# Kernel tuning notes

Hardware: AMD Instinct MI355X
Metric: run time of the kernel (lower is better)

Reference implementation:

```python
import jax, jax.numpy as jnp
import numpy as np

B = 1024      # batch of videos
T = 32768     # max snippets per video


def setup_inputs() -> dict:
    key = jax.random.key(0)
    k1, k2, k3 = jax.random.split(key, 3)
    # sigmoid-like scores in (0,1) as BCELoss expects probabilities
    scores = jax.random.uniform(k1, (B, T), dtype=jnp.float32, minval=1e-4, maxval=1.0 - 1e-4)
    label = jax.random.uniform(k2, (B,), dtype=jnp.float32)
    seqlen = jax.random.randint(k3, (B,), 1, T + 1, dtype=jnp.int32)
    return {"scores": scores, "label": label, "seqlen": seqlen}


def reference(scores, label, seqlen):
    # fwd_topk with cfg.k == -1: per-sample k_i = seqlen_i // 16 + 1,
    # mean of the top-k_i scores within the valid prefix scores[i, :seqlen_i],
    # followed by BCELoss against label.
    _, t = scores.shape
    pos = jnp.arange(t)[None, :]                      # [1, T]
    valid = pos < seqlen[:, None]                     # [B, T] ragged-length mask
    # push invalid tail to -inf so descending sort puts valid values first
    masked = jnp.where(valid, scores, -jnp.inf)
    srt = -jnp.sort(-masked, axis=1)                  # descending sort, valid prefix first
    # zero out the (-inf) tail; exactly seqlen_i leading entries are valid
    srt = jnp.where(valid, srt, 0.0)
    csum = jnp.cumsum(srt, axis=1)                    # prefix sums of sorted scores
    k = seqlen // 16 + 1                              # per-sample k, always <= seqlen
    topk_sum = jnp.take_along_axis(csum, (k - 1)[:, None], axis=1)[:, 0]
    vl_scores = topk_sum / k.astype(scores.dtype)     # mean of top-k per sample, [B]
    # BCELoss (mean reduction)
    loss = -jnp.mean(label * jnp.log(vl_scores) + (1.0 - label) * jnp.log1p(-vl_scores))
    return loss
```

## Files before the change

### kernel.cpp

```cpp
#include <hip/hip_runtime.h>
#include <math.h>

#define NB    2048
#define BLK   1024
#define NCH   256
#define CHW   (NB / NCH)
#define FIXS  1048576.0f
#define SUMMASK ((1ULL << 44) - 1)


__global__ void zero_out_kernel(float* __restrict__ out) { out[0] = 0.0f; }

__global__ __launch_bounds__(BLK) void topk_bce_kernel(
    const float* __restrict__ scores,
    const float* __restrict__ label,
    const int*   __restrict__ seqlen,
    float*       __restrict__ out,
    int T, int B)
{
    __shared__ unsigned long long hist[NB];
    __shared__ int                sc_cnt[NCH];
    __shared__ unsigned long long sc_sum[NCH];
    __shared__ int s_t, s_acc;
    __shared__ unsigned long long s_vs;

    const int row = blockIdx.x;
    const int tid = threadIdx.x;
    const int n   = seqlen[row];
    const int k   = (n >> 4) + 1;
    const float* rp   = scores + (size_t)row * (size_t)T;
    const float4* rp4 = (const float4*)rp;
    const int n4 = n >> 2;

    float lo  = 0.875f;
    float mul = 16384.0f;

    for (;;) {
        for (int i = tid; i < NB; i += BLK) hist[i] = 0ULL;
        __syncthreads();

#define PUT(x) do { \
            const float _x = (x); \
            if (_x >= lo) { \
                int _b = (int)((_x - lo) * mul); \
                if (_b > NB - 1) _b = NB - 1; \
                const unsigned int _q = (unsigned int)(_x * FIXS + 0.5f); \
                atomicAdd(&hist[_b], (1ULL << 44) | (unsigned long long)_q); \
            } \
        } while (0)

        for (int j = tid; j < n4; j += BLK) {
            float4 v = rp4[j];
            PUT(v.x); PUT(v.y); PUT(v.z); PUT(v.w);
        }
        for (int j = (n4 << 2) + tid; j < n; j += BLK) PUT(rp[j]);
#undef PUT
        __syncthreads();

        if (tid < NCH) {
            int cc = 0; unsigned long long ss = 0ULL;
            const int base = tid * CHW;
            #pragma unroll
            for (int j = 0; j < CHW; ++j) {
                const unsigned long long h = hist[base + j];
                cc += (int)(h >> 44);
                ss += (h & SUMMASK);
            }
            sc_cnt[tid] = cc; sc_sum[tid] = ss;
        }
        __syncthreads();

        for (int off = 1; off < NCH; off <<= 1) {
            int vc = 0; unsigned long long vs = 0ULL;
            if (tid < NCH) {
                vc = sc_cnt[tid]; vs = sc_sum[tid];
                if (tid + off < NCH) { vc += sc_cnt[tid + off]; vs += sc_sum[tid + off]; }
            }
            __syncthreads();
            if (tid < NCH) { sc_cnt[tid] = vc; sc_sum[tid] = vs; }
            __syncthreads();
        }

        const int total = sc_cnt[0];
        if (total >= k) break;
        lo = 0.0f; mul = (float)NB;
    }

    if (tid < NCH) {
        const int SA  = sc_cnt[tid];
        const int SAn = (tid + 1 < NCH) ? sc_cnt[tid + 1] : 0;
        if (SA >= k && SAn < k) {
            s_t   = tid;
            s_acc = SAn;
            s_vs  = (tid + 1 < NCH) ? sc_sum[tid + 1] : 0ULL;
        }
    }
    __syncthreads();

    if (tid == 0) {
        const int t = s_t;
        int acc = s_acc;
        unsigned long long vs = s_vs;
        for (int j = CHW - 1; j >= 0; --j) {
            const int bin = t * CHW + j;
            const unsigned long long h = hist[bin];
            const int c = (int)(h >> 44);
            if (acc + c >= k) {
                const int r = k - acc;
                const int m = c;
                const float sum_b  = (float)(h & SUMMASK) * (1.0f / FIXS);
                const float above  = (float)vs * (1.0f / FIXS);
                const float binw   = 1.0f / mul;
                const float bin_lo = lo + (float)bin * binw;
                float topr;
                if (r >= m) {
                    topr = sum_b;
                } else if (2 * r <= m) {
                    topr = (float)r * (bin_lo + binw)
                         - binw * (float)r * (float)(r + 1) / (2.0f * (float)(m + 1));
                } else {
                    const int q2 = m - r;
                    topr = sum_b - ((float)q2 * bin_lo
                         + binw * (float)q2 * (float)(q2 + 1) / (2.0f * (float)(m + 1)));
                }
                float v = (above + topr) / (float)k;
                v = fminf(fmaxf(v, 1e-9f), 1.0f - 1e-7f);
                const float lab  = label[row];
                const float loss = -(lab * logf(v) + (1.0f - lab) * log1pf(-v));
                atomicAdd(out, loss / (float)B);
                break;
            }
            acc += c;
            vs  += (h & SUMMASK);
        }
    }
}

extern "C" void kernel_launch(void* const* d_in, const int* in_sizes, int n_in,
                              void* d_out, int out_size, void* d_ws, size_t ws_size,
                              hipStream_t stream) {
    const float* scores = (const float*)d_in[0];
    const float* label  = (const float*)d_in[1];
    const int*   seqlen = (const int*)d_in[2];
    float* out = (float*)d_out;

    const int B = in_sizes[1];
    const int T = in_sizes[0] / B;

    zero_out_kernel<<<1, 1, 0, stream>>>(out);
    topk_bce_kernel<<<B, BLK, 0, stream>>>(scores, label, seqlen, out, T, B);
}
```

Measured before the change: 185.9 us.

## Shrink block to 512, wavefront-shuffle suffix scan, prefetch float4 loads

The block size drops to 512 threads with launch bounds allowing more resident blocks, and the chunk count doubles so each thread reduces 4 bins. The log-step shared-memory suffix scan, which needed two barriers per step, is replaced by a single-wavefront shuffle scan over 8-chunk groups. Threshold-bin selection now runs inside that wavefront without extra barriers. The streaming loop software-prefetches the next float4 before binning the current one. The aim is fewer synchronizations and better latency hiding, at the cost of fewer threads per row and a serial search within one lane.

```diff
diff --git a/kernel.cpp b/kernel.cpp
--- a/kernel.cpp
+++ b/kernel.cpp
@@ -2,16 +2,17 @@
 #include <math.h>
 
 #define NB    2048
-#define BLK   1024
-#define NCH   256
+#define BLK   512
+#define NCH   512
 #define CHW   (NB / NCH)
+#define GRP   (NCH / 64)
 #define FIXS  1048576.0f
 #define SUMMASK ((1ULL << 44) - 1)
 
 
 __global__ void zero_out_kernel(float* __restrict__ out) { out[0] = 0.0f; }
 
-__global__ __launch_bounds__(BLK) void topk_bce_kernel(
+__global__ __launch_bounds__(BLK, 8) void topk_bce_kernel(
     const float* __restrict__ scores,
     const float* __restrict__ label,
     const int*   __restrict__ seqlen,
@@ -21,8 +22,7 @@
     __shared__ unsigned long long hist[NB];
     __shared__ int                sc_cnt[NCH];
     __shared__ unsigned long long sc_sum[NCH];
-    __shared__ int s_t, s_acc;
-    __shared__ unsigned long long s_vs;
+    __shared__ int s_total;
 
     const int row = blockIdx.x;
     const int tid = threadIdx.x;
@@ -49,20 +49,28 @@
             } \
         } while (0)
 
-        for (int j = tid; j < n4; j += BLK) {
-            float4 v = rp4[j];
-            PUT(v.x); PUT(v.y); PUT(v.z); PUT(v.w);
+        {
+            int j = tid;
+            if (j < n4) {
+                float4 v = rp4[j];
+                for (int jn = j + BLK; jn < n4; jn += BLK) {
+                    float4 vn = rp4[jn];
+                    PUT(v.x); PUT(v.y); PUT(v.z); PUT(v.w);
+                    v = vn;
+                }
+                PUT(v.x); PUT(v.y); PUT(v.z); PUT(v.w);
+            }
         }
         for (int j = (n4 << 2) + tid; j < n; j += BLK) PUT(rp[j]);
 #undef PUT
         __syncthreads();
 
-        if (tid < NCH) {
+        {
             int cc = 0; unsigned long long ss = 0ULL;
             const int base = tid * CHW;
             #pragma unroll
-            for (int j = 0; j < CHW; ++j) {
-                const unsigned long long h = hist[base + j];
+            for (int c = 0; c < CHW; ++c) {
+                const unsigned long long h = hist[base + c];
                 cc += (int)(h >> 44);
                 ss += (h & SUMMASK);
             }
@@ -70,70 +78,80 @@
         }
         __syncthreads();
 
-        for (int off = 1; off < NCH; off <<= 1) {
-            int vc = 0; unsigned long long vs = 0ULL;
-            if (tid < NCH) {
-                vc = sc_cnt[tid]; vs = sc_sum[tid];
-                if (tid + off < NCH) { vc += sc_cnt[tid + off]; vs += sc_sum[tid + off]; }
+        int Ssuf = 0; unsigned long long Vsuf = 0ULL;
+        if (tid < 64) {
+            #pragma unroll
+            for (int c = 0; c < GRP; ++c) {
+                Ssuf += sc_cnt[tid * GRP + c];
+                Vsuf += sc_sum[tid * GRP + c];
             }
-            __syncthreads();
-            if (tid < NCH) { sc_cnt[tid] = vc; sc_sum[tid] = vs; }
-            __syncthreads();
+            #pragma unroll
+            for (int off = 1; off < 64; off <<= 1) {
+                int                tS = __shfl_down(Ssuf, off);
+                unsigned long long tV = __shfl_down(Vsuf, off);
+                if (tid + off < 64) { Ssuf += tS; Vsuf += tV; }
+            }
+            if (tid == 0) s_total = Ssuf;
         }
+        __syncthreads();
 
-        const int total = sc_cnt[0];
-        if (total >= k) break;
+        if (s_total >= k) {
+            if (tid < 64) {
+                int                Snext = __shfl_down(Ssuf, 1);
+                unsigned long long Vnext = __shfl_down(Vsuf, 1);
+                if (tid == 63) { Snext = 0; Vnext = 0ULL; }
+                if (Ssuf >= k && Snext < k) {
+                    int acc = Snext;
+                    unsigned long long vs = Vnext;
+                    for (int c = GRP - 1; c >= 0; --c) {
+                        const int chunk = tid * GRP + c;
+                        const int cc = sc_cnt[chunk];
+                        if (acc + cc >= k) {
+                            for (int jb = CHW - 1; jb >= 0; --jb) {
+                                const int bin = chunk * CHW + jb;
+                                const unsigned long long h = hist[bin];
+                                const int m = (int)(h >> 44);
+                                if (acc + m >= k) {
+                                    const int r = k - acc;
+                                    const float sum_b  = (float)(h & SUMMASK) * (1.0f / FIXS);
+                                    const float above  = (float)vs * (1.0f / FIXS);
+                                    const float binw   = 1.0f / mul;
+                                    const float bin_lo = lo + (float)bin * binw;
+                                    float topr;
+                                    if (r >= m) {
+                                        topr = sum_b;
+                                    } else if (2 * r <= m) {
+                                        topr = (float)r * (bin_lo + binw)
+                                             - binw * (float)r * (float)(r + 1)
+                                                    / (2.0f * (float)(m + 1));
+                                    } else {
+                                        const int q2 = m - r;
+                                        topr = sum_b - ((float)q2 * bin_lo
+                                             + binw * (float)q2 * (float)(q2 + 1)
+                                                    / (2.0f * (float)(m + 1)));
+                                    }
+                                    float v2 = (above + topr) / (float)k;
+                                    v2 = fminf(fmaxf(v2, 1e-9f), 1.0f - 1e-7f);
+                                    const float lab  = label[row];
+                                    const float loss = -(lab * logf(v2)
+                                                       + (1.0f - lab) * log1pf(-v2));
+                                    atomicAdd(out, loss / (float)B);
+                                    goto done;
+                                }
+                                acc += m;
+                                vs  += (h & SUMMASK);
+                            }
+                        }
+                        acc += cc;
+                        vs  += sc_sum[chunk];
+                    }
+                }
+            }
+            break;
+        }
         lo = 0.0f; mul = (float)NB;
     }
-
-    if (tid < NCH) {
-        const int SA  = sc_cnt[tid];
-        const int SAn = (tid + 1 < NCH) ? sc_cnt[tid + 1] : 0;
-        if (SA >= k && SAn < k) {
-            s_t   = tid;
-            s_acc = SAn;
-            s_vs  = (tid + 1 < NCH) ? sc_sum[tid + 1] : 0ULL;
-        }
-    }
-    __syncthreads();
-
-    if (tid == 0) {
-        const int t = s_t;
-        int acc = s_acc;
-        unsigned long long vs = s_vs;
-        for (int j = CHW - 1; j >= 0; --j) {
-            const int bin = t * CHW + j;
-            const unsigned long long h = hist[bin];
-            const int c = (int)(h >> 44);
-            if (acc + c >= k) {
-                const int r = k - acc;
-                const int m = c;
-                const float sum_b  = (float)(h & SUMMASK) * (1.0f / FIXS);
-                const float above  = (float)vs * (1.0f / FIXS);
-                const float binw   = 1.0f / mul;
-                const float bin_lo = lo + (float)bin * binw;
-                float topr;
-                if (r >= m) {
-                    topr = sum_b;
-                } else if (2 * r <= m) {
-                    topr = (float)r * (bin_lo + binw)
-                         - binw * (float)r * (float)(r + 1) / (2.0f * (float)(m + 1));
-                } else {
-                    const int q2 = m - r;
-                    topr = sum_b - ((float)q2 * bin_lo
-                         + binw * (float)q2 * (float)(q2 + 1) / (2.0f * (float)(m + 1)));
-                }
-                float v = (above + topr) / (float)k;
-                v = fminf(fmaxf(v, 1e-9f), 1.0f - 1e-7f);
-                const float lab  = label[row];
-                const float loss = -(lab * logf(v) + (1.0f - lab) * log1pf(-v));
-                atomicAdd(out, loss / (float)B);
-                break;
-            }
-            acc += c;
-            vs  += (h & SUMMASK);
-        }
-    }
+done: ;
 }
 
 extern "C" void kernel_launch(void* const* d_in, const int* in_sizes, int n_in,
```

Measured after the change: 185.1 us. About the same (-0.4%).
